# Performance work log

Hardware: AMD Instinct MI355X
Metric: run time of the kernel (lower is better)

## Reference

```python
import jax, jax.numpy as jnp
import numpy as np

HIDDEN = 2048
HEADS = 16
HEAD_DIM = HIDDEN // HEADS
ROPE_BASE = 10000.0


def apply_rope(x):
    # x: [B, H, S, d]  (Llama-style half-split RoPE)
    d = x.shape[-1]
    S = x.shape[-2]
    inv_freq = 1.0 / (ROPE_BASE ** (jnp.arange(0, d, 2, dtype=jnp.float32) / d))
    freqs = jnp.arange(S, dtype=jnp.float32)[:, None] * inv_freq[None, :]  # [S, d/2]
    cos = jnp.concatenate([jnp.cos(freqs), jnp.cos(freqs)], axis=-1)  # [S, d]
    sin = jnp.concatenate([jnp.sin(freqs), jnp.sin(freqs)], axis=-1)
    x1, x2 = jnp.split(x, 2, axis=-1)
    rot = jnp.concatenate([-x2, x1], axis=-1)
    return x * cos.astype(x.dtype) + rot * sin.astype(x.dtype)


def setup_inputs() -> dict:
    key = jax.random.key(0)
    ks = jax.random.split(key, 6)
    B, S = 4, 1024
    x = jax.random.normal(ks[0], (B, S, HIDDEN), dtype=jnp.float32)
    attention_mask = jnp.zeros((B, S), dtype=jnp.float32)  # additive mask
    scale = 1.0 / np.sqrt(HIDDEN)
    Wq = jax.random.normal(ks[1], (HIDDEN, HIDDEN), dtype=jnp.float32) * scale
    Wk = jax.random.normal(ks[2], (HIDDEN, HIDDEN), dtype=jnp.float32) * scale
    Wv = jax.random.normal(ks[3], (HIDDEN, HIDDEN), dtype=jnp.float32) * scale
    Wo = jax.random.normal(ks[4], (HIDDEN, HIDDEN), dtype=jnp.float32) * scale
    return {"x": x, "attention_mask": attention_mask, "Wq": Wq, "Wk": Wk, "Wv": Wv, "Wo": Wo}


def reference(x, attention_mask, Wq, Wk, Wv, Wo):
    B, S, D = x.shape
    H, d = HEADS, HEAD_DIM
    # projections (nn.Linear: y = x @ W.T, no bias)
    q = jnp.einsum('bsd,ed->bse', x, Wq).reshape(B, S, H, d).transpose(0, 2, 1, 3)
    k = jnp.einsum('bsd,ed->bse', x, Wk).reshape(B, S, H, d).transpose(0, 2, 1, 3)
    v = jnp.einsum('bsd,ed->bse', x, Wv).reshape(B, S, H, d).transpose(0, 2, 1, 3)
    q = apply_rope(q)
    k = apply_rope(k)
    scores = jnp.einsum('bhqd,bhkd->bhqk', q, k) / jnp.sqrt(jnp.float32(d))
    causal = jnp.where(jnp.tril(jnp.ones((S, S), dtype=bool)), 0.0, -jnp.inf).astype(scores.dtype)
    scores = scores + causal[None, None]
    scores = scores + attention_mask[:, None, None, :]
    attn_weights = jax.nn.softmax(scores, axis=-1)
    # dropout is identity in eval mode
    out = jnp.einsum('bhqk,bhkd->bhqd', attn_weights, v)
    out = out.transpose(0, 2, 1, 3).reshape(B, S, D)
    out = jnp.einsum('bsd,ed->bse', out, Wo)
    return (out, attn_weights)
```

## Files before the change

### kernel.cpp

```cpp
#include <hip/hip_runtime.h>
#include <hip/hip_bf16.h>


typedef __attribute__((ext_vector_type(8))) short bf16x8;
typedef __attribute__((ext_vector_type(4))) float f32x4;

#define GLD_LDS16(g, l)                                                      \
  __builtin_amdgcn_global_load_lds(                                          \
      (const __attribute__((address_space(1))) unsigned int*)(g),            \
      (__attribute__((address_space(3))) unsigned int*)(l), 16, 0, 0)

__global__ __launch_bounds__(256) void cast_kernel(
    const float* __restrict__ in, __hip_bfloat16* __restrict__ out, int n8) {
  int idx = blockIdx.x * 256 + threadIdx.x;
  if (idx >= n8) return;
  const float4* p = (const float4*)in;
  float4 a = p[idx * 2], b = p[idx * 2 + 1];
  __hip_bfloat16 h[8] = {__float2bfloat16(a.x), __float2bfloat16(a.y),
                         __float2bfloat16(a.z), __float2bfloat16(a.w),
                         __float2bfloat16(b.x), __float2bfloat16(b.y),
                         __float2bfloat16(b.z), __float2bfloat16(b.w)};
  uint4 u;
  __builtin_memcpy(&u, h, 16);
  ((uint4*)out)[idx] = u;
}

template <int MODE>
__global__ __launch_bounds__(256) void gemm_nt(
    const void* __restrict__ Abase, const __hip_bfloat16* __restrict__ Bbase,
    void* __restrict__ Cbase) {
  __shared__ alignas(16) __hip_bfloat16 lA[128][64];
  __shared__ alignas(16) __hip_bfloat16 lB[128][64];

  const int tid = threadIdx.x;
  const int m0 = blockIdx.y * 128;
  const int n0 = blockIdx.x * 128;
  const int z = blockIdx.z;

  const __hip_bfloat16* A = nullptr;
  const float* A32 = nullptr;
  const __hip_bfloat16* Bm;
  int lda = 2048, ldb = 2048, K = 2048;
  if constexpr (MODE == 0) {
    A = (const __hip_bfloat16*)Abase;
    Bm = Bbase + (size_t)z * (2048 * 2048);
  } else if constexpr (MODE == 1) {
    if (n0 > m0) return;
    int b = z >> 4, h = z & 15;
    A = (const __hip_bfloat16*)Abase + ((size_t)b * 1024) * 2048 + h * 128;
    Bm = Bbase + ((size_t)b * 1024) * 2048 + h * 128;
    K = 128;
  } else if constexpr (MODE == 2) {
    A32 = (const float*)Abase + (size_t)z * (1024 * 1024);
    Bm = Bbase + (size_t)z * (128 * 1024);
    ldb = 1024;
    K = m0 + 128;
  } else {
    A = (const __hip_bfloat16*)Abase;
    Bm = Bbase;
  }

  const int lane = tid & 63;
  const int wid = tid >> 6;
  const int wm = (wid & 1) * 64;
  const int wn = (wid >> 1) * 64;
  const int frow = lane & 15;
  const int fk = (lane >> 4) * 8;

  f32x4 acc[4][4] = {};

  for (int k0 = 0; k0 < K; k0 += 64) {
    __syncthreads();
    if constexpr (MODE == 2) {
#pragma unroll
      for (int c = 0; c < 8; ++c) {
        int lin = c * 256 + tid;
        int r = lin >> 4;
        int col = (lin & 15) << 2;
        float4 v = *(const float4*)&A32[(size_t)(m0 + r) * 1024 + k0 + col];
        __hip_bfloat16 hh[4] = {__float2bfloat16(v.x), __float2bfloat16(v.y),
                                __float2bfloat16(v.z), __float2bfloat16(v.w)};
        unsigned long long u;
        __builtin_memcpy(&u, hh, 8);
        *(unsigned long long*)&lA[r][col] = u;
      }
    } else {
#pragma unroll
      for (int c = 0; c < 4; ++c) {
        int lin = c * 256 + tid;
        int r = lin >> 3;
        int col = (lin & 7) << 3;
        GLD_LDS16(A + (size_t)(m0 + r) * lda + k0 + col, &lA[r][col]);
      }
    }
#pragma unroll
    for (int c = 0; c < 4; ++c) {
      int lin = c * 256 + tid;
      int r = lin >> 3;
      int col = (lin & 7) << 3;
      GLD_LDS16(Bm + (size_t)(n0 + r) * ldb + k0 + col, &lB[r][col]);
    }
    __syncthreads();
#pragma unroll
    for (int kk = 0; kk < 64; kk += 32) {
      bf16x8 av[4], bv[4];
#pragma unroll
      for (int i = 0; i < 4; ++i)
        av[i] = *(const bf16x8*)&lA[wm + i * 16 + frow][kk + fk];
#pragma unroll
      for (int i = 0; i < 4; ++i)
        bv[i] = *(const bf16x8*)&lB[wn + i * 16 + frow][kk + fk];
#pragma unroll
      for (int mi = 0; mi < 4; ++mi)
#pragma unroll
        for (int ni = 0; ni < 4; ++ni)
          acc[mi][ni] = __builtin_amdgcn_mfma_f32_16x16x32_bf16(
              av[mi], bv[ni], acc[mi][ni], 0, 0, 0);
    }
  }

  const int r0 = (lane >> 4) * 4;
  const int cc = lane & 15;

  if constexpr (MODE == 1) {
    float* C = (float*)Cbase + (size_t)z * (1024 * 1024);
    const float scale = 0.08838834764831845f;
#pragma unroll
    for (int mi = 0; mi < 4; ++mi)
#pragma unroll
      for (int ni = 0; ni < 4; ++ni)
#pragma unroll
        for (int r = 0; r < 4; ++r)
          C[(size_t)(m0 + wm + mi * 16 + r0 + r) * 1024 +
            (n0 + wn + ni * 16 + cc)] = acc[mi][ni][r] * scale;
  } else if constexpr (MODE == 3) {
    float* C = (float*)Cbase;
#pragma unroll
    for (int mi = 0; mi < 4; ++mi)
#pragma unroll
      for (int ni = 0; ni < 4; ++ni)
#pragma unroll
        for (int r = 0; r < 4; ++r)
          C[(size_t)(m0 + wm + mi * 16 + r0 + r) * 2048 +
            (n0 + wn + ni * 16 + cc)] = acc[mi][ni][r];
  } else if constexpr (MODE == 0) {
    __hip_bfloat16* C = (__hip_bfloat16*)Cbase + (size_t)z * (4096 * 2048);
#pragma unroll
    for (int mi = 0; mi < 4; ++mi)
#pragma unroll
      for (int ni = 0; ni < 4; ++ni)
#pragma unroll
        for (int r = 0; r < 4; ++r)
          C[(size_t)(m0 + wm + mi * 16 + r0 + r) * 2048 +
            (n0 + wn + ni * 16 + cc)] = __float2bfloat16(acc[mi][ni][r]);
  } else {
    int b = z >> 4, h = z & 15;
    __hip_bfloat16* C =
        (__hip_bfloat16*)Cbase + ((size_t)b * 1024) * 2048 + h * 128;
#pragma unroll
    for (int mi = 0; mi < 4; ++mi)
#pragma unroll
      for (int ni = 0; ni < 4; ++ni)
#pragma unroll
        for (int r = 0; r < 4; ++r)
          C[(size_t)(m0 + wm + mi * 16 + r0 + r) * 2048 +
            (n0 + wn + ni * 16 + cc)] = __float2bfloat16(acc[mi][ni][r]);
  }
}

__global__ __launch_bounds__(256) void rope_kernel(__hip_bfloat16* __restrict__ Qb,
                                                   __hip_bfloat16* __restrict__ Kb) {
  __hip_bfloat16* p = blockIdx.y ? Kb : Qb;
  int idx = blockIdx.x * 256 + threadIdx.x;
  int j = idx & 63;
  int h = (idx >> 6) & 15;
  int spos = (idx >> 10) & 1023;
  int b = idx >> 20;
  float inv_freq = __expf(-((float)(2 * j) / 128.f) * 9.210340371976184f);
  float ang = (float)spos * inv_freq;
  float c = cosf(ang), sn = sinf(ang);
  size_t base = ((size_t)(b * 1024 + spos)) * 2048 + h * 128 + j;
  float x1 = __bfloat162float(p[base]);
  float x2 = __bfloat162float(p[base + 64]);
  p[base] = __float2bfloat16(x1 * c - x2 * sn);
  p[base + 64] = __float2bfloat16(x2 * c + x1 * sn);
}

__global__ __launch_bounds__(256) void transpose_v(
    const __hip_bfloat16* __restrict__ Vb, __hip_bfloat16* __restrict__ Vt) {
  __shared__ __hip_bfloat16 t[64][65];
  int s0 = blockIdx.x * 64;
  int j0 = blockIdx.y * 64;
  int bh = blockIdx.z;
  int b = bh >> 4, h = bh & 15;
  const __hip_bfloat16* src = Vb + ((size_t)b * 1024) * 2048 + h * 128;
#pragma unroll
  for (int it = 0; it < 16; ++it) {
    int lin = it * 256 + threadIdx.x;
    int r = lin >> 6, c = lin & 63;
    t[r][c] = src[(size_t)(s0 + r) * 2048 + j0 + c];
  }
  __syncthreads();
  __hip_bfloat16* dst = Vt + ((size_t)bh * 128 + j0) * 1024 + s0;
#pragma unroll
  for (int it = 0; it < 16; ++it) {
    int lin = it * 256 + threadIdx.x;
    int r = lin >> 6, c = lin & 63;
    dst[(size_t)r * 1024 + c] = t[c][r];
  }
}

__global__ __launch_bounds__(256) void softmax_kernel(
    float* __restrict__ scores, const float* __restrict__ mask) {
  const int row = blockIdx.x;
  const int i = row & 1023;
  const int b = row >> 14;
  float* srow = scores + (size_t)row * 1024;
  const float* mrow = mask + b * 1024;
  const int tid = threadIdx.x;

  float s[4];
  float mx = -3.0e38f;
#pragma unroll
  for (int it = 0; it < 4; ++it) {
    int j = it * 256 + tid;
    float v = -3.0e38f;
    if (j <= i) v = srow[j] + mrow[j];
    s[it] = v;
    mx = fmaxf(mx, v);
  }
#pragma unroll
  for (int off = 32; off > 0; off >>= 1) mx = fmaxf(mx, __shfl_down(mx, off, 64));
  __shared__ float redm[4], reds[4];
  if ((tid & 63) == 0) redm[tid >> 6] = mx;
  __syncthreads();
  mx = fmaxf(fmaxf(redm[0], redm[1]), fmaxf(redm[2], redm[3]));

  float sum = 0.f;
#pragma unroll
  for (int it = 0; it < 4; ++it) {
    float e = (s[it] > -1.0e38f) ? __expf(s[it] - mx) : 0.f;
    s[it] = e;
    sum += e;
  }
#pragma unroll
  for (int off = 32; off > 0; off >>= 1) sum += __shfl_down(sum, off, 64);
  if ((tid & 63) == 0) reds[tid >> 6] = sum;
  __syncthreads();
  sum = reds[0] + reds[1] + reds[2] + reds[3];
  float inv = 1.0f / sum;
#pragma unroll
  for (int it = 0; it < 4; ++it) {
    int j = it * 256 + tid;
    srow[j] = s[it] * inv;
  }
}

extern "C" void kernel_launch(void* const* d_in, const int* in_sizes, int n_in,
                              void* d_out, int out_size, void* d_ws,
                              size_t ws_size, hipStream_t stream) {
  const float* x = (const float*)d_in[0];
  const float* mask = (const float*)d_in[1];
  const float* Wq = (const float*)d_in[2];
  const float* Wk = (const float*)d_in[3];
  const float* Wv = (const float*)d_in[4];
  const float* Wo = (const float*)d_in[5];
  float* out = (float*)d_out;
  float* attnw = out + (size_t)4 * 1024 * 2048;

  __hip_bfloat16* wsb = (__hip_bfloat16*)d_ws;
  __hip_bfloat16* Wob = wsb;
  __hip_bfloat16* xb  = wsb + 4194304;
  __hip_bfloat16* Wqb = wsb + 12582912;
  __hip_bfloat16* Qb  = wsb + 25165824;
  __hip_bfloat16* Kb  = wsb + 33554432;
  __hip_bfloat16* Vb  = wsb + 41943040;
  __hip_bfloat16* Vt  = wsb + 50331648;
  __hip_bfloat16* AO  = wsb + 4194304;

  cast_kernel<<<4096, 256, 0, stream>>>(x, xb, 1048576);
  cast_kernel<<<2048, 256, 0, stream>>>(Wq, Wqb, 524288);
  cast_kernel<<<2048, 256, 0, stream>>>(Wk, Wqb + 4194304, 524288);
  cast_kernel<<<2048, 256, 0, stream>>>(Wv, Wqb + 8388608, 524288);
  cast_kernel<<<2048, 256, 0, stream>>>(Wo, Wob, 524288);

  gemm_nt<0><<<dim3(16, 32, 3), 256, 0, stream>>>(xb, Wqb, Qb);
  rope_kernel<<<dim3(16384, 2), 256, 0, stream>>>(Qb, Kb);
  transpose_v<<<dim3(16, 2, 64), 256, 0, stream>>>(Vb, Vt);
  gemm_nt<1><<<dim3(8, 8, 64), 256, 0, stream>>>(Qb, Kb, attnw);
  softmax_kernel<<<65536, 256, 0, stream>>>(attnw, mask);
  gemm_nt<2><<<dim3(1, 8, 64), 256, 0, stream>>>(attnw, Vt, AO);
  gemm_nt<3><<<dim3(16, 32, 1), 256, 0, stream>>>(AO, Wob, out);
}
```

Measured before the change: 771.3 us.

## Fuse causal softmax with the PV matmul into one attention kernel

Replaces the separate row softmax kernel and the fp32-input PV GEMM with a single kernel per 128-row query tile. It first computes online row max and sum over only the causal key tiles. A second pass then writes normalized probabilities, stages them as bf16 in LDS and runs MFMA against V tiles, while explicitly zeroing the masked upper region. This cuts a kernel launch and avoids reading the fully masked upper triangle, but the scores are read twice and the grid is small and load-imbalanced across tiles.

```diff
diff --git a/kernel.cpp b/kernel.cpp
--- a/kernel.cpp
+++ b/kernel.cpp
@@ -27,8 +27,8 @@
 
 template <int MODE>
 __global__ __launch_bounds__(256) void gemm_nt(
-    const void* __restrict__ Abase, const __hip_bfloat16* __restrict__ Bbase,
-    void* __restrict__ Cbase) {
+    const __hip_bfloat16* __restrict__ Abase,
+    const __hip_bfloat16* __restrict__ Bbase, void* __restrict__ Cbase) {
   __shared__ alignas(16) __hip_bfloat16 lA[128][64];
   __shared__ alignas(16) __hip_bfloat16 lB[128][64];
 
@@ -37,26 +37,20 @@
   const int n0 = blockIdx.x * 128;
   const int z = blockIdx.z;
 
-  const __hip_bfloat16* A = nullptr;
-  const float* A32 = nullptr;
+  const __hip_bfloat16* A;
   const __hip_bfloat16* Bm;
   int lda = 2048, ldb = 2048, K = 2048;
   if constexpr (MODE == 0) {
-    A = (const __hip_bfloat16*)Abase;
+    A = Abase;
     Bm = Bbase + (size_t)z * (2048 * 2048);
   } else if constexpr (MODE == 1) {
     if (n0 > m0) return;
     int b = z >> 4, h = z & 15;
-    A = (const __hip_bfloat16*)Abase + ((size_t)b * 1024) * 2048 + h * 128;
+    A = Abase + ((size_t)b * 1024) * 2048 + h * 128;
     Bm = Bbase + ((size_t)b * 1024) * 2048 + h * 128;
     K = 128;
-  } else if constexpr (MODE == 2) {
-    A32 = (const float*)Abase + (size_t)z * (1024 * 1024);
-    Bm = Bbase + (size_t)z * (128 * 1024);
-    ldb = 1024;
-    K = m0 + 128;
   } else {
-    A = (const __hip_bfloat16*)Abase;
+    A = Abase;
     Bm = Bbase;
   }
 
@@ -71,27 +65,12 @@
 
   for (int k0 = 0; k0 < K; k0 += 64) {
     __syncthreads();
-    if constexpr (MODE == 2) {
-#pragma unroll
-      for (int c = 0; c < 8; ++c) {
-        int lin = c * 256 + tid;
-        int r = lin >> 4;
-        int col = (lin & 15) << 2;
-        float4 v = *(const float4*)&A32[(size_t)(m0 + r) * 1024 + k0 + col];
-        __hip_bfloat16 hh[4] = {__float2bfloat16(v.x), __float2bfloat16(v.y),
-                                __float2bfloat16(v.z), __float2bfloat16(v.w)};
-        unsigned long long u;
-        __builtin_memcpy(&u, hh, 8);
-        *(unsigned long long*)&lA[r][col] = u;
-      }
-    } else {
-#pragma unroll
-      for (int c = 0; c < 4; ++c) {
-        int lin = c * 256 + tid;
-        int r = lin >> 3;
-        int col = (lin & 7) << 3;
-        GLD_LDS16(A + (size_t)(m0 + r) * lda + k0 + col, &lA[r][col]);
-      }
+#pragma unroll
+    for (int c = 0; c < 4; ++c) {
+      int lin = c * 256 + tid;
+      int r = lin >> 3;
+      int col = (lin & 7) << 3;
+      GLD_LDS16(A + (size_t)(m0 + r) * lda + k0 + col, &lA[r][col]);
     }
 #pragma unroll
     for (int c = 0; c < 4; ++c) {
@@ -143,20 +122,8 @@
         for (int r = 0; r < 4; ++r)
           C[(size_t)(m0 + wm + mi * 16 + r0 + r) * 2048 +
             (n0 + wn + ni * 16 + cc)] = acc[mi][ni][r];
-  } else if constexpr (MODE == 0) {
+  } else {
     __hip_bfloat16* C = (__hip_bfloat16*)Cbase + (size_t)z * (4096 * 2048);
-#pragma unroll
-    for (int mi = 0; mi < 4; ++mi)
-#pragma unroll
-      for (int ni = 0; ni < 4; ++ni)
-#pragma unroll
-        for (int r = 0; r < 4; ++r)
-          C[(size_t)(m0 + wm + mi * 16 + r0 + r) * 2048 +
-            (n0 + wn + ni * 16 + cc)] = __float2bfloat16(acc[mi][ni][r]);
-  } else {
-    int b = z >> 4, h = z & 15;
-    __hip_bfloat16* C =
-        (__hip_bfloat16*)Cbase + ((size_t)b * 1024) * 2048 + h * 128;
 #pragma unroll
     for (int mi = 0; mi < 4; ++mi)
 #pragma unroll
@@ -210,49 +177,141 @@
   }
 }
 
-__global__ __launch_bounds__(256) void softmax_kernel(
-    float* __restrict__ scores, const float* __restrict__ mask) {
-  const int row = blockIdx.x;
-  const int i = row & 1023;
-  const int b = row >> 14;
-  float* srow = scores + (size_t)row * 1024;
+__global__ __launch_bounds__(256) void attn_pv(
+    float* __restrict__ scores, const float* __restrict__ mask,
+    const __hip_bfloat16* __restrict__ Vt, __hip_bfloat16* __restrict__ AO) {
+  __shared__ alignas(16) __hip_bfloat16 lV[128][128];
+  __shared__ alignas(16) __hip_bfloat16 lP[128][128];
+  __shared__ float sm[128], si[128];
+
+  const int tid = threadIdx.x;
+  const int lane = tid & 63;
+  const int wid = tid >> 6;
+  const int mb = blockIdx.x;
+  const int m0 = mb * 128;
+  const int z = blockIdx.y;
+  const int b = z >> 4, h = z & 15;
+
+  float* S = scores + (size_t)z * (1024 * 1024);
   const float* mrow = mask + b * 1024;
-  const int tid = threadIdx.x;
-
-  float s[4];
-  float mx = -3.0e38f;
-#pragma unroll
-  for (int it = 0; it < 4; ++it) {
-    int j = it * 256 + tid;
-    float v = -3.0e38f;
-    if (j <= i) v = srow[j] + mrow[j];
-    s[it] = v;
-    mx = fmaxf(mx, v);
-  }
-#pragma unroll
-  for (int off = 32; off > 0; off >>= 1) mx = fmaxf(mx, __shfl_down(mx, off, 64));
-  __shared__ float redm[4], reds[4];
-  if ((tid & 63) == 0) redm[tid >> 6] = mx;
+
+  const int half = lane >> 5;
+  const int csub = lane & 31;
+  for (int rr = 0; rr < 32; rr += 2) {
+    int r = wid * 32 + rr + half;
+    int i = m0 + r;
+    float m_run = -3.0e38f, s_run = 0.f;
+    for (int kt = 0; kt <= mb; ++kt) {
+      int jj = kt * 128 + csub * 4;
+      float4 s4 = *(const float4*)&S[(size_t)(m0 + r) * 1024 + jj];
+      float4 k4 = *(const float4*)&mrow[jj];
+      float v0 = (jj + 0 <= i) ? s4.x + k4.x : -3.0e38f;
+      float v1 = (jj + 1 <= i) ? s4.y + k4.y : -3.0e38f;
+      float v2 = (jj + 2 <= i) ? s4.z + k4.z : -3.0e38f;
+      float v3 = (jj + 3 <= i) ? s4.w + k4.w : -3.0e38f;
+      float tmx = fmaxf(fmaxf(v0, v1), fmaxf(v2, v3));
+      float mn = fmaxf(m_run, tmx);
+      s_run = s_run * __expf(m_run - mn);
+      s_run += (jj + 0 <= i ? __expf(v0 - mn) : 0.f) +
+               (jj + 1 <= i ? __expf(v1 - mn) : 0.f) +
+               (jj + 2 <= i ? __expf(v2 - mn) : 0.f) +
+               (jj + 3 <= i ? __expf(v3 - mn) : 0.f);
+      m_run = mn;
+    }
+#pragma unroll
+    for (int off = 1; off < 32; off <<= 1) {
+      float mo = __shfl_xor(m_run, off, 64);
+      float so = __shfl_xor(s_run, off, 64);
+      float mn = fmaxf(m_run, mo);
+      s_run = s_run * __expf(m_run - mn) + so * __expf(mo - mn);
+      m_run = mn;
+    }
+    if (csub == 0) {
+      sm[r] = m_run;
+      si[r] = 1.0f / s_run;
+    }
+  }
+
+  const int wm = (wid & 1) * 64;
+  const int wn = (wid >> 1) * 64;
+  const int frow = lane & 15;
+  const int fk = (lane >> 4) * 8;
+  f32x4 oacc[4][4] = {};
+
+  for (int kt = 0; kt <= mb; ++kt) {
+    const int c0 = kt * 128;
+    __syncthreads();
+#pragma unroll
+    for (int it = 0; it < 8; ++it) {
+      int lin = it * 256 + tid;
+      int r = lin >> 4;
+      int c = (lin & 15) << 3;
+      GLD_LDS16(Vt + ((size_t)z * 128 + r) * 1024 + c0 + c, &lV[r][c]);
+    }
+    for (int rr = 0; rr < 32; rr += 2) {
+      int r = wid * 32 + rr + half;
+      int i = m0 + r;
+      int jj = c0 + csub * 4;
+      float m_r = sm[r], iv = si[r];
+      float4 s4 = *(const float4*)&S[(size_t)(m0 + r) * 1024 + jj];
+      float4 k4 = *(const float4*)&mrow[jj];
+      float p0 = (jj + 0 <= i) ? __expf(s4.x + k4.x - m_r) * iv : 0.f;
+      float p1 = (jj + 1 <= i) ? __expf(s4.y + k4.y - m_r) * iv : 0.f;
+      float p2 = (jj + 2 <= i) ? __expf(s4.z + k4.z - m_r) * iv : 0.f;
+      float p3 = (jj + 3 <= i) ? __expf(s4.w + k4.w - m_r) * iv : 0.f;
+      *(float4*)&S[(size_t)(m0 + r) * 1024 + jj] = make_float4(p0, p1, p2, p3);
+      __hip_bfloat16 hb[4] = {__float2bfloat16(p0), __float2bfloat16(p1),
+                              __float2bfloat16(p2), __float2bfloat16(p3)};
+      unsigned long long u;
+      __builtin_memcpy(&u, hb, 8);
+      *(unsigned long long*)&lP[r][csub * 4] = u;
+    }
+    __syncthreads();
+#pragma unroll
+    for (int ks = 0; ks < 4; ++ks) {
+      bf16x8 av[4], bv[4];
+#pragma unroll
+      for (int mi = 0; mi < 4; ++mi)
+        av[mi] = *(const bf16x8*)&lP[wm + mi * 16 + frow][ks * 32 + fk];
+#pragma unroll
+      for (int ni = 0; ni < 4; ++ni)
+        bv[ni] = *(const bf16x8*)&lV[wn + ni * 16 + frow][ks * 32 + fk];
+#pragma unroll
+      for (int mi = 0; mi < 4; ++mi)
+#pragma unroll
+        for (int ni = 0; ni < 4; ++ni)
+          oacc[mi][ni] = __builtin_amdgcn_mfma_f32_16x16x32_bf16(
+              av[mi], bv[ni], oacc[mi][ni], 0, 0, 0);
+    }
+  }
+
+  {
+    const float4 z4 = make_float4(0.f, 0.f, 0.f, 0.f);
+    for (int r = 0; r < 128; ++r) {
+      for (int j = m0 + 128 + tid * 4; j < 1024; j += 1024)
+        *(float4*)&S[(size_t)(m0 + r) * 1024 + j] = z4;
+    }
+  }
+
   __syncthreads();
-  mx = fmaxf(fmaxf(redm[0], redm[1]), fmaxf(redm[2], redm[3]));
-
-  float sum = 0.f;
-#pragma unroll
-  for (int it = 0; it < 4; ++it) {
-    float e = (s[it] > -1.0e38f) ? __expf(s[it] - mx) : 0.f;
-    s[it] = e;
-    sum += e;
-  }
-#pragma unroll
-  for (int off = 32; off > 0; off >>= 1) sum += __shfl_down(sum, off, 64);
-  if ((tid & 63) == 0) reds[tid >> 6] = sum;
+  const int r0 = (lane >> 4) * 4;
+  const int cc = lane & 15;
+#pragma unroll
+  for (int mi = 0; mi < 4; ++mi)
+#pragma unroll
+    for (int ni = 0; ni < 4; ++ni)
+#pragma unroll
+      for (int r = 0; r < 4; ++r)
+        lP[wm + mi * 16 + r0 + r][wn + ni * 16 + cc] =
+            __float2bfloat16(oacc[mi][ni][r]);
   __syncthreads();
-  sum = reds[0] + reds[1] + reds[2] + reds[3];
-  float inv = 1.0f / sum;
-#pragma unroll
-  for (int it = 0; it < 4; ++it) {
-    int j = it * 256 + tid;
-    srow[j] = s[it] * inv;
+#pragma unroll
+  for (int it = 0; it < 8; ++it) {
+    int lin = it * 256 + tid;
+    int r = lin >> 4;
+    int c = (lin & 15) << 3;
+    *(uint4*)&AO[((size_t)(b * 1024) + m0 + r) * 2048 + h * 128 + c] =
+        *(const uint4*)&lP[r][c];
   }
 }
 
@@ -288,7 +347,6 @@
   rope_kernel<<<dim3(16384, 2), 256, 0, stream>>>(Qb, Kb);
   transpose_v<<<dim3(16, 2, 64), 256, 0, stream>>>(Vb, Vt);
   gemm_nt<1><<<dim3(8, 8, 64), 256, 0, stream>>>(Qb, Kb, attnw);
-  softmax_kernel<<<65536, 256, 0, stream>>>(attnw, mask);
-  gemm_nt<2><<<dim3(1, 8, 64), 256, 0, stream>>>(attnw, Vt, AO);
+  attn_pv<<<dim3(8, 64), 256, 0, stream>>>(attnw, mask, Vt, AO);
   gemm_nt<3><<<dim3(16, 32, 1), 256, 0, stream>>>(AO, Wob, out);
 }
```

Result: slower. 863.9 us (+12.0%).
